# Kernel tuning notes

Hardware: AMD Instinct MI355X
Metric: run time of the kernel (lower is better)

## Reference

```python
import jax, jax.numpy as jnp
import numpy as np

N_NODES = 100000


def gcn_conv(x, edge_index, W, b):
    """GCNConv: out = D^-1/2 (A + I) D^-1/2 (x W) + b, with added self-loops."""
    n = x.shape[0]
    xw = x @ W  # [N, C]
    loop = jnp.arange(n, dtype=edge_index.dtype)
    src = jnp.concatenate([edge_index[0], loop])  # [E+N]
    dst = jnp.concatenate([edge_index[1], loop])
    deg = jax.ops.segment_sum(jnp.ones_like(dst, dtype=xw.dtype), dst, num_segments=n)
    dinv = jax.lax.rsqrt(jnp.where(deg > 0, deg, 1.0))
    norm = dinv[src] * dinv[dst]  # [E+N]
    msgs = xw[src] * norm[:, None]  # gather + scale
    out = jax.ops.segment_sum(msgs, dst, num_segments=n)  # scatter-add
    return out + b


def setup_inputs() -> dict:
    key = jax.random.key(0)
    k1, k2, k3, k4, k5 = jax.random.split(key, 5)
    F_in, C1, C2 = 256, 64, 40
    E = 3200000
    x = jax.random.normal(k1, (N_NODES, F_in), dtype=jnp.float32)
    edge_index = jax.random.randint(k2, (2, E), 0, N_NODES, dtype=jnp.int64)
    W1 = jax.random.normal(k3, (F_in, C1), dtype=jnp.float32) / np.sqrt(F_in)
    b1 = jnp.zeros((C1,), dtype=jnp.float32)
    W2 = jax.random.normal(k4, (C1, C2), dtype=jnp.float32) / np.sqrt(C1)
    b2 = jnp.zeros((C2,), dtype=jnp.float32)
    return {"x": x, "edge_index": edge_index, "W1": W1, "b1": b1, "W2": W2, "b2": b2}


def reference(x, edge_index, W1, b1, W2, b2):
    h1 = jax.nn.relu(gcn_conv(x, edge_index, W1, b1))
    # dropout is identity in eval mode (training=False)
    h2 = gcn_conv(h1, edge_index, W2, b2)
    return jax.nn.log_softmax(h2, axis=1)
```

## Files before the change

### kernel.cpp

```cpp
#include <hip/hip_runtime.h>
#include <math.h>

#define NN 100000
#define NB 256
#define RANGE 392
#define CAP 56
#define BCAP 13824
#define NBLK_PART 512

typedef unsigned int uint;


__global__ __launch_bounds__(256) void partition_kernel(const int* __restrict__ src,
                                                        const int* __restrict__ dst,
                                                        int* __restrict__ bcur,
                                                        unsigned* __restrict__ bkt, int E) {
    __shared__ unsigned stage[NB * CAP];
    __shared__ int lcnt[NB];
    __shared__ int baseS[NB];
    for (int i = threadIdx.x; i < NB; i += 256) lcnt[i] = 0;
    __syncthreads();

    const int nq = E >> 2;
    const int stride = gridDim.x * blockDim.x;
    for (int q = blockIdx.x * blockDim.x + threadIdx.x; q < nq; q += stride) {
        const int4 s4 = ((const int4*)src)[q];
        const int4 d4 = ((const int4*)dst)[q];
#pragma unroll
        for (int k = 0; k < 4; k++) {
            const int s = (&s4.x)[k];
            const int d = (&d4.x)[k];
            const unsigned b = (unsigned)d / RANGE;
            const unsigned ent = ((unsigned)s << 9) | ((unsigned)d - b * RANGE);
            const int slot = atomicAdd(&lcnt[b], 1);
            if (slot < CAP) {
                stage[b * CAP + slot] = ent;
            } else {
                const int pos = atomicAdd(&bcur[b], 1);
                if (pos < BCAP) bkt[(size_t)b * BCAP + pos] = ent;
            }
        }
    }
    const int gid = blockIdx.x * blockDim.x + threadIdx.x;
    if (gid < (E & 3)) {
        const int e = (E & ~3) + gid;
        const int s = src[e], d = dst[e];
        const unsigned b = (unsigned)d / RANGE;
        const unsigned ent = ((unsigned)s << 9) | ((unsigned)d - b * RANGE);
        const int pos = atomicAdd(&bcur[b], 1);
        if (pos < BCAP) bkt[(size_t)b * BCAP + pos] = ent;
    }
    __syncthreads();

    if (threadIdx.x < NB) {
        const int c = min(lcnt[threadIdx.x], CAP);
        baseS[threadIdx.x] = (c > 0) ? atomicAdd(&bcur[threadIdx.x], c) : 0;
    }
    __syncthreads();

    const int w = threadIdx.x >> 6, l = threadIdx.x & 63;
    for (int b = w; b < NB; b += 4) {
        const int cnt = min(lcnt[b], CAP);
        const int base = baseS[b];
        for (int i = l; i < cnt; i += 64) {
            const int pos = base + i;
            if (pos < BCAP) bkt[(size_t)b * BCAP + pos] = stage[b * CAP + i];
        }
    }
}


__global__ __launch_bounds__(256) void bucket_sort_kernel(const int* __restrict__ bcur,
                                                          unsigned* __restrict__ bkt,
                                                          int* __restrict__ row_off,
                                                          int* __restrict__ deg,
                                                          float* __restrict__ dinv, int n) {
    __shared__ int sortedS[BCAP];
    __shared__ int cntS[RANGE];
    __shared__ int offS[RANGE];
    const int b = blockIdx.x;
    const int tid = threadIdx.x;
    unsigned* eb = bkt + (size_t)b * BCAP;
    const int m = min(bcur[b], BCAP);

    for (int i = tid; i < RANGE; i += 256) cntS[i] = 0;
    __syncthreads();
    for (int i = tid; i < m; i += 256) atomicAdd(&cntS[(int)(eb[i] & 511u)], 1);
    __syncthreads();

    if (tid < 64) {
        const int l = tid;
        int carry = 0;
        for (int base = 0; base < RANGE; base += 64) {
            const int i = base + l;
            const int c = (i < RANGE) ? cntS[i] : 0;
            int v = c;
#pragma unroll
            for (int off = 1; off < 64; off <<= 1) {
                const int t2 = __shfl_up(v, off);
                if (l >= off) v += t2;
            }
            if (i < RANGE) offS[i] = carry + v - c;
            carry += __shfl(v, 63);
        }
    }
    __syncthreads();

    for (int i = tid; i < RANGE; i += 256) {
        const int node = b * RANGE + i;
        if (node < n) {
            row_off[node] = b * BCAP + offS[i];
            deg[node] = cntS[i];
            dinv[node] = rsqrtf((float)cntS[i] + 1.0f);
        }
    }
    __syncthreads();

    for (int i = tid; i < m; i += 256) {
        const unsigned e = eb[i];
        const int pos = atomicAdd(&offS[(int)(e & 511u)], 1);
        sortedS[pos] = (int)(e >> 9);
    }
    __syncthreads();

    for (int i = tid; i < m; i += 256) eb[i] = (unsigned)sortedS[i];
}

__device__ inline uint pack_bf16(float a, float b) {
    uint ua = __float_as_uint(a), ub = __float_as_uint(b);
    ua = (ua + 0x7fffu + ((ua >> 16) & 1u)) >> 16;
    ub = (ub + 0x7fffu + ((ub >> 16) & 1u)) & 0xffff0000u;
    return ua | ub;
}
__device__ inline void acc_bf16x8(float* acc, uint4 v) {
    const uint u[4] = {v.x, v.y, v.z, v.w};
#pragma unroll
    for (int i = 0; i < 4; i++) {
        acc[2 * i]     += __uint_as_float(u[i] << 16);
        acc[2 * i + 1] += __uint_as_float(u[i] & 0xffff0000u);
    }
}


template <int K, int CREAL>
__global__ __launch_bounds__(128) void gemm_kernel(const float* __restrict__ x,
                                                   const float* __restrict__ W,
                                                   const float* __restrict__ dinv,
                                                   unsigned short* __restrict__ y, int n) {
    constexpr int KC = 32;
    constexpr int XSTR = 132;
    __shared__ float xs[KC * XSTR];
    __shared__ float ws[KC * 64];
    const int t = threadIdx.x;
    const int ct = t & 7;
    const int c0 = ct * 8;
    const int rg = t >> 3;
    const int r0 = rg * 8;
    const int row0 = blockIdx.x * 128;

    float acc[8][8];
#pragma unroll
    for (int i = 0; i < 8; i++)
#pragma unroll
        for (int j = 0; j < 8; j++) acc[i][j] = 0.f;

    for (int kc = 0; kc < K; kc += KC) {
        __syncthreads();
#pragma unroll
        for (int p = 0; p < 8; p++) {
            const int idx = t + p * 128;
            const int kq = idx & 7;
            const int row = idx >> 3;
            const int gr = min(row0 + row, n - 1);
            const float4 g = *(const float4*)(x + (size_t)gr * K + kc + kq * 4);
            xs[(kq * 4 + 0) * XSTR + row] = g.x;
            xs[(kq * 4 + 1) * XSTR + row] = g.y;
            xs[(kq * 4 + 2) * XSTR + row] = g.z;
            xs[(kq * 4 + 3) * XSTR + row] = g.w;
        }
#pragma unroll
        for (int p = 0; p < 4; p++) {
            const int idx = t + p * 128;
            const int k = idx >> 4;
            const int cq = idx & 15;
            float4 g = make_float4(0.f, 0.f, 0.f, 0.f);
            if (cq * 4 < CREAL)
                g = *(const float4*)(W + (size_t)(kc + k) * CREAL + cq * 4);
            *(float4*)(ws + k * 64 + cq * 4) = g;
        }
        __syncthreads();
#pragma unroll 4
        for (int k = 0; k < KC; k++) {
            const float4 xa = *(const float4*)(xs + k * XSTR + r0);
            const float4 xb = *(const float4*)(xs + k * XSTR + r0 + 4);
            const float4 wa = *(const float4*)(ws + k * 64 + c0);
            const float4 wb = *(const float4*)(ws + k * 64 + c0 + 4);
            const float xr[8] = {xa.x, xa.y, xa.z, xa.w, xb.x, xb.y, xb.z, xb.w};
            const float wc[8] = {wa.x, wa.y, wa.z, wa.w, wb.x, wb.y, wb.z, wb.w};
#pragma unroll
            for (int i = 0; i < 8; i++)
#pragma unroll
                for (int j = 0; j < 8; j++) acc[i][j] = fmaf(xr[i], wc[j], acc[i][j]);
        }
    }
#pragma unroll
    for (int i = 0; i < 8; i++) {
        const int row = row0 + r0 + i;
        if (row < n) {
            const float di = dinv[row];
            uint4 o;
            o.x = pack_bf16(acc[i][0] * di, acc[i][1] * di);
            o.y = pack_bf16(acc[i][2] * di, acc[i][3] * di);
            o.z = pack_bf16(acc[i][4] * di, acc[i][5] * di);
            o.w = pack_bf16(acc[i][6] * di, acc[i][7] * di);
            ((uint4*)(y + (size_t)row * 64))[ct] = o;
        }
    }
}


__global__ __launch_bounds__(256) void agg64_kernel(const unsigned short* __restrict__ y,
                                                    const int* __restrict__ row_off,
                                                    const int* __restrict__ deg,
                                                    const unsigned* __restrict__ nbr,
                                                    const float* __restrict__ dinv,
                                                    const float* __restrict__ b,
                                                    float* __restrict__ out, int n) {
    int node = blockIdx.x * 4 + (threadIdx.x >> 6);
    if (node >= n) return;
    const int l = threadIdx.x & 63;
    const int g = l >> 3;
    const int cq = l & 7;

    const int start = row_off[node];
    const int dg = deg[node];

    float acc[8];
#pragma unroll
    for (int i = 0; i < 8; i++) acc[i] = 0.f;

    for (int base = 0; base < dg; base += 64) {
        const int m = min(64, dg - base);
        const int idx = (l < m) ? (int)nbr[start + base + l] : 0;
        for (int j0 = 0; j0 < m; j0 += 16) {
            const int jA = j0 + g;
            const int jB = j0 + 8 + g;
            const int sA = __shfl(idx, jA);
            const int sB = __shfl(idx, jB);
            const bool okA = jA < m;
            const bool okB = jB < m;
            uint4 vA = ((const uint4*)(y + (size_t)sA * 64))[cq];
            uint4 vB = ((const uint4*)(y + (size_t)sB * 64))[cq];
            vA.x = okA ? vA.x : 0u; vA.y = okA ? vA.y : 0u;
            vA.z = okA ? vA.z : 0u; vA.w = okA ? vA.w : 0u;
            vB.x = okB ? vB.x : 0u; vB.y = okB ? vB.y : 0u;
            vB.z = okB ? vB.z : 0u; vB.w = okB ? vB.w : 0u;
            acc_bf16x8(acc, vA);
            acc_bf16x8(acc, vB);
        }
    }
#pragma unroll
    for (int off = 8; off < 64; off <<= 1)
#pragma unroll
        for (int i = 0; i < 8; i++) acc[i] += __shfl_xor(acc[i], off);

    float self[8];
#pragma unroll
    for (int i = 0; i < 8; i++) self[i] = 0.f;
    acc_bf16x8(self, ((const uint4*)(y + (size_t)node * 64))[cq]);
    const float di = dinv[node];
    const float4 bv0 = *(const float4*)(b + cq * 8);
    const float4 bv1 = *(const float4*)(b + cq * 8 + 4);
    const float bb[8] = {bv0.x, bv0.y, bv0.z, bv0.w, bv1.x, bv1.y, bv1.z, bv1.w};
    if (l < 8) {
        float4 o0, o1;
        o0.x = fmaxf((acc[0] + self[0]) * di + bb[0], 0.f);
        o0.y = fmaxf((acc[1] + self[1]) * di + bb[1], 0.f);
        o0.z = fmaxf((acc[2] + self[2]) * di + bb[2], 0.f);
        o0.w = fmaxf((acc[3] + self[3]) * di + bb[3], 0.f);
        o1.x = fmaxf((acc[4] + self[4]) * di + bb[4], 0.f);
        o1.y = fmaxf((acc[5] + self[5]) * di + bb[5], 0.f);
        o1.z = fmaxf((acc[6] + self[6]) * di + bb[6], 0.f);
        o1.w = fmaxf((acc[7] + self[7]) * di + bb[7], 0.f);
        *(float4*)(out + (size_t)node * 64 + l * 8) = o0;
        *(float4*)(out + (size_t)node * 64 + l * 8 + 4) = o1;
    }
}


__global__ __launch_bounds__(256) void agg40_lsm_kernel(const unsigned short* __restrict__ y,
                                                        const int* __restrict__ row_off,
                                                        const int* __restrict__ deg,
                                                        const unsigned* __restrict__ nbr,
                                                        const float* __restrict__ dinv,
                                                        const float* __restrict__ b,
                                                        float* __restrict__ out, int n) {
    int node = blockIdx.x * 4 + (threadIdx.x >> 6);
    if (node >= n) return;
    const int l = threadIdx.x & 63;
    const int g = l >> 3;
    const int cq = l & 7;
    const bool real = (cq < 5);

    const int start = row_off[node];
    const int dg = deg[node];

    float acc[8];
#pragma unroll
    for (int i = 0; i < 8; i++) acc[i] = 0.f;

    for (int base = 0; base < dg; base += 64) {
        const int m = min(64, dg - base);
        const int idx = (l < m) ? (int)nbr[start + base + l] : 0;
        for (int j0 = 0; j0 < m; j0 += 16) {
            const int jA = j0 + g;
            const int jB = j0 + 8 + g;
            const int sA = __shfl(idx, jA);
            const int sB = __shfl(idx, jB);
            const bool okA = jA < m;
            const bool okB = jB < m;
            uint4 vA = ((const uint4*)(y + (size_t)sA * 64))[cq];
            uint4 vB = ((const uint4*)(y + (size_t)sB * 64))[cq];
            vA.x = okA ? vA.x : 0u; vA.y = okA ? vA.y : 0u;
            vA.z = okA ? vA.z : 0u; vA.w = okA ? vA.w : 0u;
            vB.x = okB ? vB.x : 0u; vB.y = okB ? vB.y : 0u;
            vB.z = okB ? vB.z : 0u; vB.w = okB ? vB.w : 0u;
            acc_bf16x8(acc, vA);
            acc_bf16x8(acc, vB);
        }
    }
#pragma unroll
    for (int off = 8; off < 64; off <<= 1)
#pragma unroll
        for (int i = 0; i < 8; i++) acc[i] += __shfl_xor(acc[i], off);

    float self[8];
#pragma unroll
    for (int i = 0; i < 8; i++) self[i] = 0.f;
    acc_bf16x8(self, ((const uint4*)(y + (size_t)node * 64))[cq]);
    const float di = dinv[node];
    float bb[8];
#pragma unroll
    for (int i = 0; i < 8; i++) bb[i] = 0.f;
    if (real) {
        const float4 bv0 = *(const float4*)(b + cq * 8);
        const float4 bv1 = *(const float4*)(b + cq * 8 + 4);
        bb[0] = bv0.x; bb[1] = bv0.y; bb[2] = bv0.z; bb[3] = bv0.w;
        bb[4] = bv1.x; bb[5] = bv1.y; bb[6] = bv1.z; bb[7] = bv1.w;
    }
    float h[8];
#pragma unroll
    for (int i = 0; i < 8; i++) h[i] = (acc[i] + self[i]) * di + bb[i];

    float mx = -INFINITY;
    if (real)
#pragma unroll
        for (int i = 0; i < 8; i++) mx = fmaxf(mx, h[i]);
#pragma unroll
    for (int off = 1; off < 8; off <<= 1) mx = fmaxf(mx, __shfl_xor(mx, off));
    float es = 0.f;
    if (real)
#pragma unroll
        for (int i = 0; i < 8; i++) es += __expf(h[i] - mx);
#pragma unroll
    for (int off = 1; off < 8; off <<= 1) es += __shfl_xor(es, off);
    const float ls = mx + __logf(es);

    if (l < 5) {
        float4 o0, o1;
        o0.x = h[0] - ls; o0.y = h[1] - ls; o0.z = h[2] - ls; o0.w = h[3] - ls;
        o1.x = h[4] - ls; o1.y = h[5] - ls; o1.z = h[6] - ls; o1.w = h[7] - ls;
        *(float4*)(out + (size_t)node * 40 + l * 8) = o0;
        *(float4*)(out + (size_t)node * 40 + l * 8 + 4) = o1;
    }
}


extern "C" void kernel_launch(void* const* d_in, const int* in_sizes, int n_in,
                              void* d_out, int out_size, void* d_ws, size_t ws_size,
                              hipStream_t stream) {
    const float* x  = (const float*)d_in[0];
    const int* edges = (const int*)d_in[1];
    const float* W1 = (const float*)d_in[2];
    const float* b1 = (const float*)d_in[3];
    const float* W2 = (const float*)d_in[4];
    const float* b2 = (const float*)d_in[5];
    float* out = (float*)d_out;

    const int n = NN;
    const int E = in_sizes[1] / 2;

    char* ws = (char*)d_ws;
    size_t off = 0;
    auto alloc = [&](size_t bytes) -> void* {
        void* p = ws + off;
        off += (bytes + 255) & ~(size_t)255;
        return p;
    };
    int*            bcur    = (int*)alloc((size_t)NB * 4);
    unsigned*       bkt     = (unsigned*)alloc((size_t)NB * BCAP * 4);
    int*            row_off = (int*)alloc((size_t)n * 4);
    int*            deg     = (int*)alloc((size_t)n * 4);
    float*          dinv    = (float*)alloc((size_t)n * 4);
    float*          h1      = (float*)alloc((size_t)n * 64 * 4);
    unsigned short* y1      = (unsigned short*)alloc((size_t)n * 64 * 2);
    unsigned short* y2      = y1;

    const int* src = edges;
    const int* dst = edges + E;

    hipMemsetAsync(bcur, 0, (size_t)NB * 4, stream);
    partition_kernel<<<NBLK_PART, 256, 0, stream>>>(src, dst, bcur, bkt, E);
    bucket_sort_kernel<<<NB, 256, 0, stream>>>(bcur, bkt, row_off, deg, dinv, n);

    const int gblk = (n + 127) / 128;

    gemm_kernel<256, 64><<<gblk, 128, 0, stream>>>(x, W1, dinv, y1, n);
    agg64_kernel<<<(n + 3) / 4, 256, 0, stream>>>(y1, row_off, deg, bkt, dinv, b1, h1, n);

    gemm_kernel<64, 40><<<gblk, 128, 0, stream>>>(h1, W2, dinv, y2, n);
    agg40_lsm_kernel<<<(n + 3) / 4, 256, 0, stream>>>(y2, row_off, deg, bkt, dinv, b2, out, n);
}
```

Before: 393.5 us.

## Replace scalar FMA GEMM with bf16 MFMA GEMM and register prefetch

Rewrites the dense x@W kernel to convert inputs and weights to bf16 and compute 16x16x32 tiles with MFMA instructions on 256-thread blocks. The whole weight matrix is staged transposed in shared memory, and the next K-chunk of x is prefetched into registers while the current one is computed. The aim is to cut the FP32 FMA cost of the two GEMMs, trading it for bf16 rounding of inputs before accumulation, which slightly changes numerics. Output is still scaled by dinv and stored as bf16, but now as scattered 2-byte stores.

```diff
diff --git a/kernel.cpp b/kernel.cpp
--- a/kernel.cpp
+++ b/kernel.cpp
@@ -9,6 +9,8 @@
 #define NBLK_PART 512
 
 typedef unsigned int uint;
+typedef __attribute__((ext_vector_type(8))) short short8;
+typedef __attribute__((ext_vector_type(4))) float f32x4;
 
 
 __global__ __launch_bounds__(256) void partition_kernel(const int* __restrict__ src,
@@ -132,6 +134,10 @@
     ub = (ub + 0x7fffu + ((ub >> 16) & 1u)) & 0xffff0000u;
     return ua | ub;
 }
+__device__ inline unsigned short bf16r(float f) {
+    uint u = __float_as_uint(f);
+    return (unsigned short)((u + 0x7fffu + ((u >> 16) & 1u)) >> 16);
+}
 __device__ inline void acc_bf16x8(float* acc, uint4 v) {
     const uint u[4] = {v.x, v.y, v.z, v.w};
 #pragma unroll
@@ -143,77 +149,98 @@
 
 
 template <int K, int CREAL>
-__global__ __launch_bounds__(128) void gemm_kernel(const float* __restrict__ x,
-                                                   const float* __restrict__ W,
-                                                   const float* __restrict__ dinv,
-                                                   unsigned short* __restrict__ y, int n) {
-    constexpr int KC = 32;
-    constexpr int XSTR = 132;
-    __shared__ float xs[KC * XSTR];
-    __shared__ float ws[KC * 64];
+__global__ __launch_bounds__(256) void gemm_mfma_kernel(const float* __restrict__ x,
+                                                        const float* __restrict__ W,
+                                                        const float* __restrict__ dinv,
+                                                        unsigned short* __restrict__ y,
+                                                        int n) {
+    constexpr int KP = K + 8;
+    __shared__ unsigned short wt[64 * KP];
+    __shared__ unsigned short as[128 * 40];
     const int t = threadIdx.x;
-    const int ct = t & 7;
-    const int c0 = ct * 8;
-    const int rg = t >> 3;
-    const int r0 = rg * 8;
+    const int l = t & 63;
+    const int w = t >> 6;
+    const int lane15 = l & 15;
+    const int quad = l >> 4;
     const int row0 = blockIdx.x * 128;
 
-    float acc[8][8];
-#pragma unroll
-    for (int i = 0; i < 8; i++)
-#pragma unroll
-        for (int j = 0; j < 8; j++) acc[i][j] = 0.f;
-
-    for (int kc = 0; kc < K; kc += KC) {
+    for (int idx = t; idx < K * 16; idx += 256) {
+        const int k = idx >> 4;
+        const int c4 = (idx & 15) * 4;
+        float4 g = make_float4(0.f, 0.f, 0.f, 0.f);
+        if (c4 < CREAL) g = *(const float4*)(W + (size_t)k * CREAL + c4);
+        wt[(c4 + 0) * KP + k] = bf16r(g.x);
+        wt[(c4 + 1) * KP + k] = bf16r(g.y);
+        wt[(c4 + 2) * KP + k] = bf16r(g.z);
+        wt[(c4 + 3) * KP + k] = bf16r(g.w);
+    }
+
+    f32x4 acc[2][4];
+#pragma unroll
+    for (int mt = 0; mt < 2; mt++)
+#pragma unroll
+        for (int nt = 0; nt < 4; nt++) acc[mt][nt] = (f32x4){0.f, 0.f, 0.f, 0.f};
+
+    float4 g[4];
+#pragma unroll
+    for (int p = 0; p < 4; p++) {
+        const int idx = t + p * 256;
+        const int row = idx >> 3;
+        const int kq = idx & 7;
+        const int gr = min(row0 + row, n - 1);
+        g[p] = *(const float4*)(x + (size_t)gr * K + kq * 4);
+    }
+
+    for (int kc = 0; kc < K; kc += 32) {
         __syncthreads();
 #pragma unroll
-        for (int p = 0; p < 8; p++) {
-            const int idx = t + p * 128;
+        for (int p = 0; p < 4; p++) {
+            const int idx = t + p * 256;
+            const int row = idx >> 3;
             const int kq = idx & 7;
-            const int row = idx >> 3;
-            const int gr = min(row0 + row, n - 1);
-            const float4 g = *(const float4*)(x + (size_t)gr * K + kc + kq * 4);
-            xs[(kq * 4 + 0) * XSTR + row] = g.x;
-            xs[(kq * 4 + 1) * XSTR + row] = g.y;
-            xs[(kq * 4 + 2) * XSTR + row] = g.z;
-            xs[(kq * 4 + 3) * XSTR + row] = g.w;
-        }
-#pragma unroll
-        for (int p = 0; p < 4; p++) {
-            const int idx = t + p * 128;
-            const int k = idx >> 4;
-            const int cq = idx & 15;
-            float4 g = make_float4(0.f, 0.f, 0.f, 0.f);
-            if (cq * 4 < CREAL)
-                g = *(const float4*)(W + (size_t)(kc + k) * CREAL + cq * 4);
-            *(float4*)(ws + k * 64 + cq * 4) = g;
+            uint2 pk;
+            pk.x = pack_bf16(g[p].x, g[p].y);
+            pk.y = pack_bf16(g[p].z, g[p].w);
+            *(uint2*)(as + row * 40 + kq * 4) = pk;
+        }
+        if (kc + 32 < K) {
+#pragma unroll
+            for (int p = 0; p < 4; p++) {
+                const int idx = t + p * 256;
+                const int row = idx >> 3;
+                const int kq = idx & 7;
+                const int gr = min(row0 + row, n - 1);
+                g[p] = *(const float4*)(x + (size_t)gr * K + kc + 32 + kq * 4);
+            }
         }
         __syncthreads();
-#pragma unroll 4
-        for (int k = 0; k < KC; k++) {
-            const float4 xa = *(const float4*)(xs + k * XSTR + r0);
-            const float4 xb = *(const float4*)(xs + k * XSTR + r0 + 4);
-            const float4 wa = *(const float4*)(ws + k * 64 + c0);
-            const float4 wb = *(const float4*)(ws + k * 64 + c0 + 4);
-            const float xr[8] = {xa.x, xa.y, xa.z, xa.w, xb.x, xb.y, xb.z, xb.w};
-            const float wc[8] = {wa.x, wa.y, wa.z, wa.w, wb.x, wb.y, wb.z, wb.w};
-#pragma unroll
-            for (int i = 0; i < 8; i++)
-#pragma unroll
-                for (int j = 0; j < 8; j++) acc[i][j] = fmaf(xr[i], wc[j], acc[i][j]);
-        }
-    }
-#pragma unroll
-    for (int i = 0; i < 8; i++) {
-        const int row = row0 + r0 + i;
-        if (row < n) {
-            const float di = dinv[row];
-            uint4 o;
-            o.x = pack_bf16(acc[i][0] * di, acc[i][1] * di);
-            o.y = pack_bf16(acc[i][2] * di, acc[i][3] * di);
-            o.z = pack_bf16(acc[i][4] * di, acc[i][5] * di);
-            o.w = pack_bf16(acc[i][6] * di, acc[i][7] * di);
-            ((uint4*)(y + (size_t)row * 64))[ct] = o;
+
+        short8 bf[4];
+#pragma unroll
+        for (int nt = 0; nt < 4; nt++)
+            bf[nt] = *(const short8*)(wt + (nt * 16 + lane15) * KP + kc + quad * 8);
+#pragma unroll
+        for (int mt = 0; mt < 2; mt++) {
+            const short8 af =
+                *(const short8*)(as + (w * 32 + mt * 16 + lane15) * 40 + quad * 8);
+#pragma unroll
+            for (int nt = 0; nt < 4; nt++)
+                acc[mt][nt] =
+                    __builtin_amdgcn_mfma_f32_16x16x32_bf16(af, bf[nt], acc[mt][nt], 0, 0, 0);
+        }
+    }
+
+#pragma unroll
+    for (int mt = 0; mt < 2; mt++) {
+#pragma unroll
+        for (int r = 0; r < 4; r++) {
+            const int row = row0 + w * 32 + mt * 16 + quad * 4 + r;
+            if (row < n) {
+                const float di = dinv[row];
+#pragma unroll
+                for (int nt = 0; nt < 4; nt++)
+                    y[(size_t)row * 64 + nt * 16 + lane15] = bf16r(acc[mt][nt][r] * di);
+            }
         }
     }
 }
@@ -415,9 +442,9 @@
 
     const int gblk = (n + 127) / 128;
 
-    gemm_kernel<256, 64><<<gblk, 128, 0, stream>>>(x, W1, dinv, y1, n);
+    gemm_mfma_kernel<256, 64><<<gblk, 256, 0, stream>>>(x, W1, dinv, y1, n);
     agg64_kernel<<<(n + 3) / 4, 256, 0, stream>>>(y1, row_off, deg, bkt, dinv, b1, h1, n);
 
-    gemm_kernel<64, 40><<<gblk, 128, 0, stream>>>(h1, W2, dinv, y2, n);
+    gemm_mfma_kernel<64, 40><<<gblk, 256, 0, stream>>>(h1, W2, dinv, y2, n);
     agg40_lsm_kernel<<<(n + 3) / 4, 256, 0, stream>>>(y2, row_off, deg, bkt, dinv, b2, out, n);
 }
```

New measurement: 367.0 us. 6.7% less time.
